# Performance work log

Hardware: AMD Instinct MI355X
Metric: run time of the kernel (lower is better)

The kernel has to match this reference:

```python
import jax, jax.numpy as jnp
import numpy as np

B, T, D, H = 2, 4096, 1024, 16
DK, DV, C = 64, 128, 64  # head_k_dim, head_v_dim, chunk size


def setup_inputs() -> dict:
    key = jax.random.key(0)
    ks = jax.random.split(key, 7)
    std = 0.02
    return {
        "x": jax.random.normal(ks[0], (B, T, D), jnp.float32),
        "Wq": jax.random.normal(ks[1], (D, D), jnp.float32) * std,
        "Wk": jax.random.normal(ks[2], (D, D), jnp.float32) * std,
        "Wv": jax.random.normal(ks[3], (D, 2 * D), jnp.float32) * std,
        "Wg": jax.random.normal(ks[4], (D, 2 * D), jnp.float32) * std,
        "Wo": jax.random.normal(ks[5], (2 * D, D), jnp.float32) * std,
        "g_norm_w": jnp.ones((DV,), jnp.float32),
    }


def _rope(q, k):  # q,k: [B,T,H,DK], neox-style rotate-half rotary
    dk = q.shape[-1]
    inv = 1.0 / (10000.0 ** (jnp.arange(0, dk, 2, dtype=jnp.float32) / dk))
    t = jnp.arange(q.shape[1], dtype=jnp.float32)
    f = t[:, None] * inv[None, :]                      # [T, dk/2]
    cos = jnp.cos(f)[None, :, None, :]
    sin = jnp.sin(f)[None, :, None, :]
    def rot(x):
        x1, x2 = jnp.split(x, 2, axis=-1)
        return jnp.concatenate([x1 * cos - x2 * sin, x1 * sin + x2 * cos], -1)
    return rot(q), rot(k)


def reference(x, Wq, Wk, Wv, Wg, Wo, g_norm_w):
    b, t, _ = x.shape
    nc = t // C
    q = (x @ Wq).reshape(b, t, H, DK)
    k = (x @ Wk).reshape(b, t, H, DK)
    v = (x @ Wv).reshape(b, t, H, DV)
    g = (x @ Wg).reshape(b, t, H, DV)
    q, k = _rope(q, k)
    q = q * (DK ** -0.5)

    # per-head retention decay: gamma_h = 1 - 2^(-5-h)
    gamma = 1.0 - jnp.exp2(-5.0 - jnp.arange(H, dtype=jnp.float32))  # [H]
    i = jnp.arange(C, dtype=jnp.float32)
    dq = gamma[:, None] ** (i + 1.0)          # [H,C] cross-chunk decay on q
    dkv = gamma[:, None] ** (C - 1.0 - i)     # [H,C] decay of k into state
    rel = i[:, None] - i[None, :]
    Dmat = jnp.where(rel >= 0, gamma[:, None, None] ** jnp.maximum(rel, 0.0), 0.0)  # [H,C,C]
    gC = gamma ** C

    to_chunks = lambda a: a.reshape(b, nc, C, H, a.shape[-1]).transpose(1, 0, 3, 2, 4)
    qc, kc, vc = to_chunks(q), to_chunks(k), to_chunks(v)  # [NC,B,H,C,d]

    def step(S, inp):
        qi, ki, vi = inp
        o_inter = jnp.einsum('bhcd,bhde->bhce', qi * dq[None, :, :, None], S)
        A = jnp.einsum('bhid,bhjd->bhij', qi, ki) * Dmat[None]
        o_intra = jnp.einsum('bhij,bhje->bhie', A, vi)
        S = gC[None, :, None, None] * S + jnp.einsum('bhjd,bhje->bhde', ki * dkv[None, :, :, None], vi)
        return S, o_inter + o_intra

    S0 = jnp.zeros((b, H, DK, DV), x.dtype)
    _, o = jax.lax.scan(step, S0, (qc, kc, vc))            # [NC,B,H,C,DV]
    o = o.transpose(1, 0, 3, 2, 4).reshape(b, t, H, DV)

    # fused per-head RMSNorm + swish gate
    rms = o * jax.lax.rsqrt(jnp.mean(o * o, axis=-1, keepdims=True) + 1e-5) * g_norm_w
    o = rms * (g * jax.nn.sigmoid(g))
    return o.reshape(b, t, H * DV) @ Wo
```

## Files before the change

kernel.cpp:

```cpp
#include <hip/hip_runtime.h>
#include <stdint.h>
#include <type_traits>

typedef unsigned short u16;
typedef __attribute__((ext_vector_type(8))) short short8;
typedef __attribute__((ext_vector_type(4))) float f32x4;

#define MFMA16(a,b,c) __builtin_amdgcn_mfma_f32_16x16x32_bf16(a,b,c,0,0,0)

__device__ __forceinline__ u16 f2bf(float f){
  uint32_t u = __builtin_bit_cast(uint32_t, f);
  u += 0x7FFFu + ((u>>16)&1u);
  return (u16)(u>>16);
}
__device__ __forceinline__ float bf2f(u16 h){
  uint32_t u = ((uint32_t)h)<<16;
  return __builtin_bit_cast(float, u);
}

__global__ __launch_bounds__(256) void prep(const float* __restrict__ x, u16* __restrict__ xb,
    const float* __restrict__ Wq, const float* __restrict__ Wk, const float* __restrict__ Wv,
    const float* __restrict__ Wg, const float* __restrict__ Wo,
    u16* __restrict__ WcatT, u16* __restrict__ WoT){
  int bid = blockIdx.x;
  if (bid < 8192){
    int i = (bid*256 + threadIdx.x)*4;
    float4 v = *(const float4*)&x[i];
    uint2 u;
    u.x = (uint32_t)f2bf(v.x) | ((uint32_t)f2bf(v.y)<<16);
    u.y = (uint32_t)f2bf(v.z) | ((uint32_t)f2bf(v.w)<<16);
    *(uint2*)&xb[i] = u;
    return;
  }
  bid -= 8192;
  const float* src; u16* dst; int R, Cc, tc, tr;
  if (bid < 1024){        src=Wq; dst=WcatT;             R=1024; Cc=1024; int b=bid;      tc=(b&31)*32; tr=(b>>5)*32; }
  else if (bid < 2048){   src=Wk; dst=WcatT+1024*1024;   R=1024; Cc=1024; int b=bid-1024; tc=(b&31)*32; tr=(b>>5)*32; }
  else if (bid < 4096){   src=Wv; dst=WcatT+2048*1024;   R=1024; Cc=2048; int b=bid-2048; tc=(b&63)*32; tr=(b>>6)*32; }
  else if (bid < 6144){   src=Wg; dst=WcatT+4096*1024;   R=1024; Cc=2048; int b=bid-4096; tc=(b&63)*32; tr=(b>>6)*32; }
  else {                  src=Wo; dst=WoT;               R=2048; Cc=1024; int b=bid-6144; tc=(b&31)*32; tr=(b>>5)*32; }
  __shared__ float tile[32][33];
  int lr = threadIdx.x>>5, lc = threadIdx.x&31;
  #pragma unroll
  for (int p=0;p<4;p++)
    tile[lr+p*8][lc] = src[(size_t)(tr+lr+p*8)*Cc + tc + lc];
  __syncthreads();
  #pragma unroll
  for (int p=0;p<4;p++)
    dst[(size_t)(tc+lr+p*8)*R + tr + lc] = f2bf(tile[lc][lr+p*8]);
}

__global__ __launch_bounds__(512,1) void gemm1_256(const u16* __restrict__ A,
    const u16* __restrict__ BT, u16* __restrict__ C){
  __shared__ u16 L[4*16384];
  const int bm = blockIdx.y, bn = blockIdx.x;
  const int t = threadIdx.x;
  const int w = t>>6, l = t&63;
  const int wm = w>>2, wn = w&3;
  const int lr = l&15, lg = l>>4;
  const int srow = t>>2;
  const int gsw = ((t&3) - (t>>3)) & 3;
  const size_t aoff = (size_t)(bm*256 + srow)*1024 + gsw*8;
  const size_t boff = (size_t)(bn*256 + srow)*1024 + gsw*8;
  const int sdo = t*8;

  u16 *p0 = L, *p1 = L+16384, *p2 = L+32768, *p3 = L+49152;

  auto STAGE = [&](u16* buf, int k0){
    __builtin_amdgcn_global_load_lds(&A[aoff + k0],                     buf + sdo,               16,0,0);
    __builtin_amdgcn_global_load_lds(&A[aoff + (size_t)128*1024 + k0],  buf + sdo + 4096,        16,0,0);
    __builtin_amdgcn_global_load_lds(&BT[boff + k0],                    buf + 8192 + sdo,        16,0,0);
    __builtin_amdgcn_global_load_lds(&BT[boff + (size_t)128*1024 + k0], buf + 8192 + sdo + 4096, 16,0,0);
  };

  f32x4 acc[8][4];
  #pragma unroll
  for (int m=0;m<8;m++)
    #pragma unroll
    for (int n=0;n<4;n++) acc[m][n] = (f32x4){0.f,0.f,0.f,0.f};

  STAGE(p0, 0); STAGE(p1, 32); STAGE(p2, 64);
  for (int kt=0; kt<32; ++kt){
    if      (kt < 30) asm volatile("s_waitcnt vmcnt(8)" ::: "memory");
    else if (kt == 30) asm volatile("s_waitcnt vmcnt(4)" ::: "memory");
    else               asm volatile("s_waitcnt vmcnt(0)" ::: "memory");
    __builtin_amdgcn_s_barrier();
    if (kt+3 < 32) STAGE(p3, (kt+3)*32);
    short8 af[8], bf4[4];
    #pragma unroll
    for (int m=0;m<8;m++){
      int row = wm*128 + m*16 + lr;
      af[m] = *(const short8*)(p0 + row*32 + (((lg + (row>>1))&3)<<3));
    }
    #pragma unroll
    for (int n=0;n<4;n++){
      int row = wn*64 + n*16 + lr;
      bf4[n] = *(const short8*)(p0 + 8192 + row*32 + (((lg + (row>>1))&3)<<3));
    }
    __builtin_amdgcn_s_setprio(1);
    #pragma unroll
    for (int m=0;m<8;m++)
      #pragma unroll
      for (int n=0;n<4;n++)
        acc[m][n] = MFMA16(af[m], bf4[n], acc[m][n]);
    __builtin_amdgcn_s_setprio(0);
    { u16* tp=p0; p0=p1; p1=p2; p2=p3; p3=tp; }
  }

  __syncthreads();
  const bool qk = (bn < 8);
  const float qscale = (bn < 4) ? 0.125f : 1.0f;
  #pragma unroll
  for (int s=0;s<4;++s){
    if (wm == (s>>1)){
      #pragma unroll
      for (int mm=0;mm<4;++mm){
        const int m = (s&1)*4 + mm;
        if (qk){
          #pragma unroll
          for (int n=0;n<2;n++){
            float inv = exp2f((float)(n*16+lr) * (-13.287712379549449f/32.0f));
            #pragma unroll
            for (int r=0;r<4;r++){
              int grow = bm*256 + wm*128 + m*16 + lg*4 + r;
              float f = (float)(grow & 4095) * inv;
              float sn, cs; __sincosf(f, &sn, &cs);
              float x1 = acc[m][n][r], x2 = acc[m][n+2][r];
              int lrow = mm*16 + lg*4 + r;
              L[lrow*264 + wn*64 + n*16 + lr]     = f2bf((x1*cs - x2*sn)*qscale);
              L[lrow*264 + wn*64 + (n+2)*16 + lr] = f2bf((x1*sn + x2*cs)*qscale);
            }
          }
        } else {
          #pragma unroll
          for (int n=0;n<4;n++)
            #pragma unroll
            for (int r=0;r<4;r++)
              L[(mm*16+lg*4+r)*264 + wn*64 + n*16 + lr] = f2bf(acc[m][n][r]);
        }
      }
    }
    __syncthreads();
    #pragma unroll
    for (int p=0;p<4;p++){
      int idx = p*512 + t;
      int row = idx>>5, gr = idx&31;
      *(short8*)&C[(size_t)(bm*256 + s*64 + row)*6144 + bn*256 + gr*8] =
        *(const short8*)&L[row*264 + gr*8];
    }
    __syncthreads();
  }
}

__global__ __launch_bounds__(256) void gemm2_nt(const u16* __restrict__ A,
    const u16* __restrict__ BT, float* __restrict__ C, int M, int N, int K){
  __shared__ u16 L[3*8192];
  const int bm = blockIdx.y, bn = blockIdx.x;
  const int t = threadIdx.x;
  const int w = t>>6, l = t&63;
  const int wr = (w>>1)*64, wc = (w&1)*64;
  const int lr = l&15, lg = l>>4;
  const int srow = t>>2;
  const int gsw  = ((t&3) - (t>>3)) & 3;
  const int scol = gsw*8;
  const size_t aoff = (size_t)(bm*128 + srow)*K + scol;
  const size_t boff = (size_t)(bn*128 + srow)*K + scol;
  const int sdo = t*8;

  u16 *a0 = L,          *b0 = L + 4096;
  u16 *a1 = L + 8192,   *b1 = L + 12288;
  u16 *a2 = L + 16384,  *b2 = L + 20480;

  auto STAGE = [&](u16* la, u16* lb, int k0){
    __builtin_amdgcn_global_load_lds(&A[aoff + k0],                 la + sdo,        16, 0, 0);
    __builtin_amdgcn_global_load_lds(&A[aoff + (size_t)64*K + k0],  la + sdo + 2048, 16, 0, 0);
    __builtin_amdgcn_global_load_lds(&BT[boff + k0],                lb + sdo,        16, 0, 0);
    __builtin_amdgcn_global_load_lds(&BT[boff + (size_t)64*K + k0], lb + sdo + 2048, 16, 0, 0);
  };

  f32x4 acc[4][4];
  for (int m=0;m<4;m++) for (int n=0;n<4;n++) acc[m][n] = (f32x4){0.f,0.f,0.f,0.f};

  const int NT = K >> 5;
  STAGE(a0, b0, 0);
  STAGE(a1, b1, 32);
  for (int kt=0; kt<NT; ++kt){
    if (kt < NT-1) asm volatile("s_waitcnt vmcnt(4)" ::: "memory");
    else           asm volatile("s_waitcnt vmcnt(0)" ::: "memory");
    __builtin_amdgcn_s_barrier();
    if (kt+2 < NT) STAGE(a2, b2, (kt+2)*32);
    short8 af[4], bfr[4];
    #pragma unroll
    for (int m=0;m<4;m++){
      int rrow = wr + m*16 + lr;
      af[m]  = *(const short8*)(a0 + rrow*32 + (((lg + (rrow>>1))&3)<<3));
    }
    #pragma unroll
    for (int n=0;n<4;n++){
      int rrow = wc + n*16 + lr;
      bfr[n] = *(const short8*)(b0 + rrow*32 + (((lg + (rrow>>1))&3)<<3));
    }
    __builtin_amdgcn_s_setprio(1);
    #pragma unroll
    for (int m=0;m<4;m++)
      #pragma unroll
      for (int n=0;n<4;n++)
        acc[m][n] = MFMA16(af[m], bfr[n], acc[m][n]);
    __builtin_amdgcn_s_setprio(0);
    { u16* tp=a0; a0=a1; a1=a2; a2=tp; }
    { u16* tp=b0; b0=b1; b1=b2; b2=tp; }
  }

  #pragma unroll
  for (int m=0;m<4;m++)
    #pragma unroll
    for (int n=0;n<4;n++){
    int row = bm*128 + wr + m*16 + lg*4;
    int col = bn*128 + wc + n*16 + lr;
    #pragma unroll
    for (int r=0;r<4;r++)
      C[(size_t)(row+r)*N + col] = acc[m][n][r];
  }
}

__global__ __launch_bounds__(256) void retention_r1(const u16* __restrict__ qkvg,
    u16* __restrict__ o, u16* __restrict__ states){
  int bid = blockIdx.x;
  int c = bid & 63, h = (bid>>6)&15, b = bid>>10;
  int t = threadIdx.x, w = t>>6, l = t&63, lr = l&15, lg = l>>4;
  __shared__ u16 SH[17280];
  __shared__ float pw[72];
  u16* kT    = SH;
  u16* vT    = SH + 4096;
  u16* A_lds = SH + 12288;
  float log2g = log2f(1.0f - exp2f(-5.0f - (float)h));
  if (t < 65) pw[t] = exp2f(log2g*(float)t);
  const size_t rowbase = (size_t)(b*4096 + c*64);
  __syncthreads();

  {
    int rp = t>>3, cg = t&7;
    int r0 = rp*2;
    short8 k0v = *(const short8*)&qkvg[(rowbase+r0  )*6144 + 1024 + h*64 + cg*8];
    short8 k1v = *(const short8*)&qkvg[(rowbase+r0+1)*6144 + 1024 + h*64 + cg*8];
    float d0 = pw[63-r0], d1 = pw[62-r0];
    #pragma unroll
    for (int j=0;j<8;j++){
      int d = cg*8+j;
      uint32_t pk = (uint32_t)f2bf(bf2f((u16)k0v[j])*d0) | ((uint32_t)f2bf(bf2f((u16)k1v[j])*d1)<<16);
      *(uint32_t*)&kT[d*64 + (((r0>>3) ^ (d>>3))<<3) + (r0&7)] = pk;
    }
    #pragma unroll
    for (int p=0;p<2;p++){
      int it = t + p*256;
      int vrp = it>>4, vcg = it&15;
      int vr0 = vrp*2;
      short8 v0 = *(const short8*)&qkvg[(rowbase+vr0  )*6144 + 2048 + h*128 + vcg*8];
      short8 v1 = *(const short8*)&qkvg[(rowbase+vr0+1)*6144 + 2048 + h*128 + vcg*8];
      #pragma unroll
      for (int j=0;j<8;j++){
        int e = vcg*8+j;
        uint32_t pv = (uint32_t)(u16)v0[j] | ((uint32_t)(u16)v1[j]<<16);
        *(uint32_t*)&vT[e*64 + (((vr0>>3) ^ ((e>>3)&7))<<3) + (vr0&7)] = pv;
      }
    }
  }

  f32x4 z4 = {0.f,0.f,0.f,0.f};
  f32x4 accA[4] = {z4,z4,z4,z4};
  #pragma unroll
  for (int ks=0;ks<2;ks++){
    short8 aq = *(const short8*)&qkvg[(rowbase + w*16+lr)*6144 + h*64 + ks*32 + lg*8];
    #pragma unroll
    for (int n=0;n<4;n++){
      short8 bk = *(const short8*)&qkvg[(rowbase + n*16+lr)*6144 + 1024 + h*64 + ks*32 + lg*8];
      accA[n] = MFMA16(aq, bk, accA[n]);
    }
  }
  #pragma unroll
  for (int n=0;n<4;n++)
    #pragma unroll
    for (int r=0;r<4;r++){
    int i = w*16 + lg*4 + r, j = n*16 + lr;
    float v = (i>=j) ? accA[n][r]*pw[i-j] : 0.0f;
    A_lds[i*72 + j] = f2bf(v);
  }
  __syncthreads();

  f32x4 accO[8], accS[8];
  #pragma unroll
  for (int n=0;n<8;n++){ accO[n]=z4; accS[n]=z4; }
  #pragma unroll
  for (int ks=0;ks<2;ks++){
    int rk = w*16+lr;
    short8 aA = *(const short8*)&A_lds[rk*72 + ks*32+lg*8];
    short8 aK = *(const short8*)&kT[rk*64 + (((ks*4+lg) ^ (rk>>3))<<3)];
    #pragma unroll
    for (int n=0;n<8;n++){
      int e2 = n*16+lr;
      short8 bv = *(const short8*)&vT[e2*64 + (((ks*4+lg) ^ ((e2>>3)&7))<<3)];
      accO[n] = MFMA16(aA, bv, accO[n]);
      accS[n] = MFMA16(aK, bv, accS[n]);
    }
  }

  __syncthreads();
  u16* oB = SH;
  u16* sB = SH + 8448;
  #pragma unroll
  for (int n=0;n<8;n++)
    #pragma unroll
    for (int r=0;r<4;r++){
    int i = w*16 + lg*4 + r, e = n*16 + lr;
    oB[i*132 + e] = f2bf(accO[n][r]);
    sB[e*68 + i]  = f2bf(accS[n][r]);
  }
  __syncthreads();
  const size_t ob = rowbase*2048 + h*128;
  const size_t sb = ((size_t)(b*16+h)*64 + c)*8192;
  {
    int orow = t>>2, ocol = (t&3)*32;
    #pragma unroll
    for (int q=0;q<4;q++)
      *(short8*)&o[ob + (size_t)orow*2048 + ocol + q*8] = *(const short8*)&oB[orow*132 + ocol + q*8];
    int se = t>>1, sd = (t&1)*32;
    #pragma unroll
    for (int q=0;q<4;q++)
      *(short8*)&states[sb + (size_t)se*64 + sd + q*8] = *(const short8*)&sB[se*68 + sd + q*8];
  }
}

__global__ __launch_bounds__(256) void retention_r2(const u16* __restrict__ qkvg,
    const u16* __restrict__ states, u16* __restrict__ o){
  int bid = blockIdx.x;
  int vblk = bid & 7, h = (bid>>3)&15, b = bid>>7;
  int t = threadIdx.x, w = t>>6, l = t&63, lr = l&15, lg = l>>4;
  int e0 = vblk*16;
  float log2g = log2f(1.0f - exp2f(-5.0f - (float)h));
  float gC = exp2f(64.0f*log2g);
  float dqv[4];
  #pragma unroll
  for (int r=0;r<4;r++) dqv[r] = exp2f(log2g*(float)(w*16 + lg*4 + r + 1));
  float st[16];
  #pragma unroll
  for (int i=0;i<16;i++) st[i]=0.f;
  const size_t sbase = ((size_t)(b*16+h)*64)*8192 + (size_t)(e0+lr)*64 + lg*8;
  const size_t qb = (size_t)(b*4096)*6144 + h*64 + (size_t)(w*16+lr)*6144 + lg*8;
  const size_t obh = (size_t)(b*4096)*2048 + h*128 + e0 + lr;
  short8 nsc0 = *(const short8*)&states[sbase];
  short8 nsc1 = *(const short8*)&states[sbase + 32];
  short8 naq0 = *(const short8*)&qkvg[qb];
  short8 naq1 = *(const short8*)&qkvg[qb + 32];
  for (int c=0;c<64;c++){
    short8 sc0 = nsc0, sc1 = nsc1, aq0 = naq0, aq1 = naq1;
    if (c < 63){
      nsc0 = *(const short8*)&states[sbase + (size_t)(c+1)*8192];
      nsc1 = *(const short8*)&states[sbase + (size_t)(c+1)*8192 + 32];
      naq0 = *(const short8*)&qkvg[qb + (size_t)(c+1)*64*6144];
      naq1 = *(const short8*)&qkvg[qb + (size_t)(c+1)*64*6144 + 32];
    }
    f32x4 acc = {0.f,0.f,0.f,0.f};
    short8 bs0, bs1;
    #pragma unroll
    for (int dd=0;dd<8;dd++) bs0[dd] = (short)f2bf(st[dd]);
    #pragma unroll
    for (int dd=0;dd<8;dd++) bs1[dd] = (short)f2bf(st[dd+8]);
    acc = MFMA16(aq0, bs0, acc);
    acc = MFMA16(aq1, bs1, acc);
    #pragma unroll
    for (int r=0;r<4;r++){
      int i = w*16 + lg*4 + r;
      size_t oi = obh + (size_t)(c*64 + i)*2048;
      o[oi] = f2bf(bf2f(o[oi]) + dqv[r]*acc[r]);
    }
    #pragma unroll
    for (int i2=0;i2<8;i2++) st[i2]   = gC*st[i2]   + bf2f((u16)sc0[i2]);
    #pragma unroll
    for (int i2=0;i2<8;i2++) st[i2+8] = gC*st[i2+8] + bf2f((u16)sc1[i2]);
  }
}

__global__ __launch_bounds__(256) void norm_gate(const u16* __restrict__ o,
    const u16* __restrict__ qkvg, const float* __restrict__ gnw, u16* __restrict__ og){
  int rowh = blockIdx.x*4 + (threadIdx.x>>6);
  int l = threadIdx.x & 63;
  int row = rowh >> 4, h = rowh & 15;
  uint32_t vv = *(const uint32_t*)(o + (size_t)row*2048 + h*128 + l*2);
  float v0 = bf2f((u16)(vv&0xFFFF)), v1 = bf2f((u16)(vv>>16));
  float ss = v0*v0 + v1*v1;
  #pragma unroll
  for (int off=32; off; off>>=1) ss += __shfl_xor(ss, off);
  float rs = rsqrtf(ss*(1.0f/128.0f) + 1e-5f);
  uint32_t gg = *(const uint32_t*)(qkvg + (size_t)row*6144 + 4096 + h*128 + l*2);
  float g0 = bf2f((u16)(gg&0xFFFF)), g1 = bf2f((u16)(gg>>16));
  float r0 = v0*rs*gnw[l*2]   * (g0/(1.f+expf(-g0)));
  float r1 = v1*rs*gnw[l*2+1] * (g1/(1.f+expf(-g1)));
  uint32_t pack = (uint32_t)f2bf(r0) | ((uint32_t)f2bf(r1)<<16);
  *(uint32_t*)(og + (size_t)row*2048 + h*128 + l*2) = pack;
}

extern "C" void kernel_launch(void* const* d_in, const int* in_sizes, int n_in,
                              void* d_out, int out_size, void* d_ws, size_t ws_size,
                              hipStream_t stream){
  const float* x   = (const float*)d_in[0];
  const float* Wq  = (const float*)d_in[1];
  const float* Wk  = (const float*)d_in[2];
  const float* Wv  = (const float*)d_in[3];
  const float* Wg  = (const float*)d_in[4];
  const float* Wo  = (const float*)d_in[5];
  const float* gnw = (const float*)d_in[6];
  float* out = (float*)d_out;

  const size_t NEED = 171966464ull;
  if (ws_size < NEED) return;

  char* base = (char*)d_ws;
  u16* qkvg  = (u16*)(base);
  u16* obuf  = (u16*)(base + 100663296);
  u16* WoT   = (u16*)(base + 134217728);
  u16* xb    = (u16*)(base + 138412032);
  u16* WcatT = (u16*)(base + 155189248);
  u16* stt   = (u16*)(base + 138412032);
  u16* og    = (u16*)(base + 138412032);

  prep<<<16384,256,0,stream>>>(x, xb, Wq, Wk, Wv, Wg, Wo, WcatT, WoT);
  gemm1_256<<<dim3(24,32),512,0,stream>>>(xb, WcatT, qkvg);
  retention_r1<<<2048,256,0,stream>>>(qkvg, obuf, stt);
  retention_r2<<<256,256,0,stream>>>(qkvg, stt, obuf);
  norm_gate<<<32768,256,0,stream>>>(obuf, qkvg, gnw, og);
  gemm2_nt<<<dim3(8,64),256,0,stream>>>(og, WoT, out, 8192, 1024, 2048);
}
```

Before: 306.2 us.

## Split GEMM k-step into two phases interleaving LDS reads, prefetch and MFMA

Restructures the main loop of the projection GEMM into two half-phases. Each phase loads half the A fragments from LDS, issues half of the next-stage global-to-LDS prefetch (A then B), and runs its half of the MFMAs, with extra s_barrier and sched_barrier fences. The goal is to spread memory traffic across the compute and overlap LDS reads with MFMA work across waves, similar to ping-pong scheduling. In exchange it adds more workgroup barriers per iteration. The vmcnt accounting stays at the same four loads per stage, just issued in a different order.

```diff
diff --git a/kernel.cpp b/kernel.cpp
--- a/kernel.cpp
+++ b/kernel.cpp
@@ -66,9 +66,11 @@
 
   u16 *p0 = L, *p1 = L+16384, *p2 = L+32768, *p3 = L+49152;
 
-  auto STAGE = [&](u16* buf, int k0){
+  auto STAGE_A = [&](u16* buf, int k0){
     __builtin_amdgcn_global_load_lds(&A[aoff + k0],                     buf + sdo,               16,0,0);
     __builtin_amdgcn_global_load_lds(&A[aoff + (size_t)128*1024 + k0],  buf + sdo + 4096,        16,0,0);
+  };
+  auto STAGE_B = [&](u16* buf, int k0){
     __builtin_amdgcn_global_load_lds(&BT[boff + k0],                    buf + 8192 + sdo,        16,0,0);
     __builtin_amdgcn_global_load_lds(&BT[boff + (size_t)128*1024 + k0], buf + 8192 + sdo + 4096, 16,0,0);
   };
@@ -79,16 +81,18 @@
     #pragma unroll
     for (int n=0;n<4;n++) acc[m][n] = (f32x4){0.f,0.f,0.f,0.f};
 
-  STAGE(p0, 0); STAGE(p1, 32); STAGE(p2, 64);
+  STAGE_A(p0, 0);  STAGE_B(p0, 0);
+  STAGE_A(p1, 32); STAGE_B(p1, 32);
+  STAGE_A(p2, 64); STAGE_B(p2, 64);
   for (int kt=0; kt<32; ++kt){
     if      (kt < 30) asm volatile("s_waitcnt vmcnt(8)" ::: "memory");
     else if (kt == 30) asm volatile("s_waitcnt vmcnt(4)" ::: "memory");
     else               asm volatile("s_waitcnt vmcnt(0)" ::: "memory");
     __builtin_amdgcn_s_barrier();
-    if (kt+3 < 32) STAGE(p3, (kt+3)*32);
+    __builtin_amdgcn_sched_barrier(0);
     short8 af[8], bf4[4];
     #pragma unroll
-    for (int m=0;m<8;m++){
+    for (int m=0;m<4;m++){
       int row = wm*128 + m*16 + lr;
       af[m] = *(const short8*)(p0 + row*32 + (((lg + (row>>1))&3)<<3));
     }
@@ -97,9 +101,29 @@
       int row = wn*64 + n*16 + lr;
       bf4[n] = *(const short8*)(p0 + 8192 + row*32 + (((lg + (row>>1))&3)<<3));
     }
+    if (kt+3 < 32) STAGE_A(p3, (kt+3)*32);
+    __builtin_amdgcn_s_barrier();
+    __builtin_amdgcn_sched_barrier(0);
     __builtin_amdgcn_s_setprio(1);
     #pragma unroll
-    for (int m=0;m<8;m++)
+    for (int m=0;m<4;m++)
+      #pragma unroll
+      for (int n=0;n<4;n++)
+        acc[m][n] = MFMA16(af[m], bf4[n], acc[m][n]);
+    __builtin_amdgcn_s_setprio(0);
+    __builtin_amdgcn_s_barrier();
+    __builtin_amdgcn_sched_barrier(0);
+    #pragma unroll
+    for (int m=4;m<8;m++){
+      int row = wm*128 + m*16 + lr;
+      af[m] = *(const short8*)(p0 + row*32 + (((lg + (row>>1))&3)<<3));
+    }
+    if (kt+3 < 32) STAGE_B(p3, (kt+3)*32);
+    __builtin_amdgcn_s_barrier();
+    __builtin_amdgcn_sched_barrier(0);
+    __builtin_amdgcn_s_setprio(1);
+    #pragma unroll
+    for (int m=4;m<8;m++)
       #pragma unroll
       for (int n=0;n<4;n++)
         acc[m][n] = MFMA16(af[m], bf4[n], acc[m][n]);
```

Result: no change. 309.2 us (+1.0%).
